# Kernel optimization log

Measured on AMD Instinct MI355X. Metric: run time of the kernel, lower is better.

Reference implementation:

```python
import jax, jax.numpy as jnp
import numpy as np

N_HEAD = 16
N_KV_GROUP = 4
WINDOW = 256


def setup_inputs() -> dict:
    key = jax.random.key(0)
    ks = jax.random.split(key, 5)
    B, T, C = 2, 2048, 1024
    KV = C // N_HEAD * N_KV_GROUP  # 256
    s = 0.02
    return {
        "x": jax.random.normal(ks[0], (B, T, C), jnp.float32),
        "Wq": jax.random.normal(ks[1], (C, C), jnp.float32) * s,
        "bq": jnp.zeros((C,), jnp.float32),
        "Wk": jax.random.normal(ks[2], (C, KV), jnp.float32) * s,
        "bk": jnp.zeros((KV,), jnp.float32),
        "Wv": jax.random.normal(ks[3], (C, KV), jnp.float32) * s,
        "bv": jnp.zeros((KV,), jnp.float32),
        "Wo": jax.random.normal(ks[4], (C, C), jnp.float32) * s,
        "bo": jnp.zeros((C,), jnp.float32),
    }


def reference(x, Wq, bq, Wk, bk, Wv, bv, Wo, bo):
    B, T, C = x.shape
    hd = C // N_HEAD  # head dim = 64
    n_rep = N_HEAD // N_KV_GROUP

    q = x @ Wq + bq                      # [B,T,C]
    k = x @ Wk + bk                      # [B,T,KV]
    v = x @ Wv + bv

    q = q.reshape(B, T, N_HEAD, hd).transpose(0, 2, 1, 3)       # [B,H,T,d]
    k = k.reshape(B, T, N_KV_GROUP, hd).transpose(0, 2, 1, 3)   # [B,G,T,d]
    v = v.reshape(B, T, N_KV_GROUP, hd).transpose(0, 2, 1, 3)

    # GQA: repeat_interleave kv heads along head dim
    k_rep = jnp.repeat(k, n_rep, axis=1)                         # [B,H,T,d]
    v_rep = jnp.repeat(v, n_rep, axis=1)

    att = jnp.einsum("bhqd,bhkd->bhqk", q, k_rep) / jnp.sqrt(jnp.float32(hd))

    # causal + sliding window band mask: q position i attends to j in [i-WINDOW, i]
    i = jnp.arange(T)[:, None]
    j = jnp.arange(T)[None, :]
    band = (j <= i) & (j >= i - WINDOW)                           # [T,T]
    att = jnp.where(band[None, None], att, jnp.float32(-jnp.inf))

    att = jax.nn.softmax(att, axis=-1)
    y = jnp.einsum("bhqk,bhkd->bhqd", att, v_rep)                 # [B,H,T,d]
    y = y.transpose(0, 2, 1, 3).reshape(B, T, C)
    return y @ Wo + bo
```

## Files before the change

kernel.cpp:

```cpp
#include <hip/hip_runtime.h>
#include <hip/hip_bf16.h>

#define TT 2048
#define CC 1024
#define KVD 256
#define QKVD 1536

typedef __bf16 bf16x8 __attribute__((ext_vector_type(8)));
typedef float f32x4 __attribute__((ext_vector_type(4)));

__device__ __forceinline__ void gload_lds16(const __hip_bfloat16* g, __hip_bfloat16* l) {
  __builtin_amdgcn_global_load_lds(
      (const __attribute__((address_space(1))) unsigned int*)g,
      (__attribute__((address_space(3))) unsigned int*)l, 16, 0, 0);
}


__global__ __launch_bounds__(256) void k_prep(const float* __restrict__ x,
                                              const float* __restrict__ Wq,
                                              const float* __restrict__ Wk,
                                              const float* __restrict__ Wv,
                                              const float* __restrict__ Wo,
                                              const float* __restrict__ bq,
                                              const float* __restrict__ bk,
                                              const float* __restrict__ bv,
                                              __hip_bfloat16* __restrict__ xbf,
                                              __hip_bfloat16* __restrict__ wqkvT,
                                              __hip_bfloat16* __restrict__ woT,
                                              float* __restrict__ bqkv) {
  const int bxid = blockIdx.x;
  if (bxid < 4096) {
    size_t idx = ((size_t)bxid * 256 + threadIdx.x) * 4;
    float4 v = *(const float4*)(x + idx);
    xbf[idx + 0] = __float2bfloat16(v.x);
    xbf[idx + 1] = __float2bfloat16(v.y);
    xbf[idx + 2] = __float2bfloat16(v.z);
    xbf[idx + 3] = __float2bfloat16(v.w);
    return;
  }
  if (bxid == 4736) {
    for (int i = threadIdx.x; i < 1536; i += 256) {
      float v;
      if (i < 1024)      v = bq[i];
      else if (i < 1280) v = bk[i - 1024];
      else               v = bv[i - 1280];
      bqkv[i] = v;
    }
    return;
  }
  __shared__ float tile[64][65];
  const float* src;
  int ncols, k0, n0;
  __hip_bfloat16* dst;
  if (bxid < 4480) {
    const int idx = bxid - 4096;
    k0 = (idx & 15) * 64;
    n0 = (idx >> 4) * 64;
    dst = wqkvT;
    if (n0 < 1024)      { src = Wq; ncols = 1024; }
    else if (n0 < 1280) { src = Wk - 1024; ncols = 256; }
    else                { src = Wv - 1280; ncols = 256; }
  } else {
    const int idx = bxid - 4480;
    k0 = (idx & 15) * 64;
    n0 = (idx >> 4) * 64;
    dst = woT; src = Wo; ncols = 1024;
  }
  const int rw = threadIdx.x >> 6;
  const int cl = threadIdx.x & 63;
#pragma unroll
  for (int i = 0; i < 16; ++i) {
    const int kr = rw + i * 4;
    tile[kr][cl] = src[(size_t)(k0 + kr) * ncols + n0 + cl];
  }
  __syncthreads();
#pragma unroll
  for (int i = 0; i < 16; ++i) {
    const int nr = rw + i * 4;
    dst[(size_t)(n0 + nr) * 1024 + k0 + cl] = __float2bfloat16(tile[cl][nr]);
  }
}


__global__ __launch_bounds__(256, 3) void k_gemm1(const __hip_bfloat16* __restrict__ A,
                                                  const __hip_bfloat16* __restrict__ BT,
                                                  const float* __restrict__ bias,
                                                  __hip_bfloat16* __restrict__ C,
                                                  __hip_bfloat16* __restrict__ vtg) {
  __shared__ __hip_bfloat16 As[128][64];
  __shared__ __hip_bfloat16 Bs[128][64];

  const int tid  = threadIdx.x;
  const int m0   = blockIdx.y * 128;
  const int n0   = blockIdx.x * 128;
  const int w    = tid >> 6;
  const int lane = tid & 63;
  const int quad = lane >> 4;
  const int l16  = lane & 15;
  const int wm   = (w >> 1) * 64;
  const int wn   = (w & 1) * 64;

  const int dl_r = lane >> 3;
  const int dl_c = (lane & 7) ^ dl_r;

  const __hip_bfloat16* gA = A + (size_t)(m0 + w * 32 + dl_r) * 1024 + dl_c * 8;
  const __hip_bfloat16* gB = BT + (size_t)(n0 + w * 32 + dl_r) * 1024 + dl_c * 8;

  f32x4 acc[4][4] = {};

  for (int kt = 0; kt < 16; ++kt) {
    const int k0 = kt << 6;
#pragma unroll
    for (int rr = 0; rr < 4; ++rr) {
      gload_lds16(gA + k0 + (size_t)(rr * 8) * 1024, &As[w * 32 + rr * 8][0]);
      gload_lds16(gB + k0 + (size_t)(rr * 8) * 1024, &Bs[w * 32 + rr * 8][0]);
    }
    __syncthreads();

#pragma unroll
    for (int ks = 0; ks < 2; ++ks) {
      const int cb = (ks << 2) + quad;
      bf16x8 fa[4], fb[4];
#pragma unroll
      for (int i = 0; i < 4; ++i)
        fa[i] = *(const bf16x8*)&As[wm + i * 16 + l16][(cb ^ (l16 & 7)) << 3];
#pragma unroll
      for (int j = 0; j < 4; ++j)
        fb[j] = *(const bf16x8*)&Bs[wn + j * 16 + l16][(cb ^ (l16 & 7)) << 3];
#pragma unroll
      for (int i = 0; i < 4; ++i)
#pragma unroll
        for (int j = 0; j < 4; ++j)
          acc[i][j] = __builtin_amdgcn_mfma_f32_16x16x32_bf16(fa[i], fb[j], acc[i][j], 0, 0, 0);
    }
    __syncthreads();
  }

#pragma unroll
  for (int j = 0; j < 4; ++j) {
    const int gn = n0 + wn + j * 16 + l16;
    const float bias_v = bias[gn];
    if (gn >= 1280) {
      const int dfull = gn - 1280;
      const int gg = dfull >> 6;
      const int dd = dfull & 63;
#pragma unroll
      for (int i = 0; i < 4; ++i) {
        const int gm = m0 + wm + i * 16 + quad * 4;
        const int bb = gm >> 11;
        const int tl = gm & 2047;
        __hip_bfloat16 tmp[4];
#pragma unroll
        for (int r = 0; r < 4; ++r) tmp[r] = __float2bfloat16(acc[i][j][r] + bias_v);
        *(uint2*)(vtg + ((size_t)((bb * 4 + gg) * 64 + dd)) * TT + tl) = *(const uint2*)tmp;
      }
    } else {
#pragma unroll
      for (int i = 0; i < 4; ++i) {
        const int gmb = m0 + wm + i * 16 + quad * 4;
#pragma unroll
        for (int r = 0; r < 4; ++r)
          C[(size_t)(gmb + r) * QKVD + gn] = __float2bfloat16(acc[i][j][r] + bias_v);
      }
    }
  }
}


__global__ __launch_bounds__(256, 4) void k_gemm2(const __hip_bfloat16* __restrict__ A,
                                                  const __hip_bfloat16* __restrict__ BT,
                                                  const float* __restrict__ bias,
                                                  float* __restrict__ C) {
  __shared__ __hip_bfloat16 As[64][64];
  __shared__ __hip_bfloat16 Bs[128][64];

  const int tid  = threadIdx.x;
  const int m0   = blockIdx.y * 64;
  const int n0   = blockIdx.x * 128;
  const int w    = tid >> 6;
  const int lane = tid & 63;
  const int quad = lane >> 4;
  const int l16  = lane & 15;
  const int wm   = (w >> 1) * 32;
  const int wn   = (w & 1) * 64;

  const int dl_r = lane >> 3;
  const int dl_c = (lane & 7) ^ dl_r;

  const __hip_bfloat16* gA = A + (size_t)(m0 + w * 16 + dl_r) * 1024 + dl_c * 8;
  const __hip_bfloat16* gB = BT + (size_t)(n0 + w * 32 + dl_r) * 1024 + dl_c * 8;

  f32x4 acc[2][4] = {};

  for (int kt = 0; kt < 16; ++kt) {
    const int k0 = kt << 6;
    gload_lds16(gA + k0,                     &As[w * 16][0]);
    gload_lds16(gA + k0 + (size_t)8 * 1024,  &As[w * 16 + 8][0]);
    gload_lds16(gB + k0,                     &Bs[w * 32][0]);
    gload_lds16(gB + k0 + (size_t)8 * 1024,  &Bs[w * 32 + 8][0]);
    gload_lds16(gB + k0 + (size_t)16 * 1024, &Bs[w * 32 + 16][0]);
    gload_lds16(gB + k0 + (size_t)24 * 1024, &Bs[w * 32 + 24][0]);
    __syncthreads();

#pragma unroll
    for (int ks = 0; ks < 2; ++ks) {
      const int cb = (ks << 2) + quad;
      bf16x8 fa[2], fb[4];
#pragma unroll
      for (int i = 0; i < 2; ++i)
        fa[i] = *(const bf16x8*)&As[wm + i * 16 + l16][(cb ^ (l16 & 7)) << 3];
#pragma unroll
      for (int j = 0; j < 4; ++j)
        fb[j] = *(const bf16x8*)&Bs[wn + j * 16 + l16][(cb ^ (l16 & 7)) << 3];
#pragma unroll
      for (int i = 0; i < 2; ++i)
#pragma unroll
        for (int j = 0; j < 4; ++j)
          acc[i][j] = __builtin_amdgcn_mfma_f32_16x16x32_bf16(fa[i], fb[j], acc[i][j], 0, 0, 0);
    }
    __syncthreads();
  }

#pragma unroll
  for (int j = 0; j < 4; ++j) {
    const int gn = n0 + wn + j * 16 + l16;
    const float bias_v = bias[gn];
#pragma unroll
    for (int i = 0; i < 2; ++i) {
      const int gmb = m0 + wm + i * 16 + quad * 4;
#pragma unroll
      for (int r = 0; r < 4; ++r)
        C[(size_t)(gmb + r) * CC + gn] = acc[i][j][r] + bias_v;
    }
  }
}


__global__ __launch_bounds__(256) void k_attn(const __hip_bfloat16* __restrict__ qkv,
                                              const __hip_bfloat16* __restrict__ vtg,
                                              __hip_bfloat16* __restrict__ y) {
  __shared__ __hip_bfloat16 Kb[2][64][64];
  __shared__ __hip_bfloat16 Vb[2][64][64];
  __shared__ __hip_bfloat16 Ps[4][16][72];

  const int t    = threadIdx.x;
  const int w    = t >> 6;
  const int lane = t & 63;
  const int quad = lane >> 4;
  const int l16  = lane & 15;
  const int bx   = blockIdx.x;
  const int h    = blockIdx.y;
  const int b    = blockIdx.z;
  const int g    = h >> 2;
  const int i0   = bx * 64;
  const int qrow      = i0 + w * 16 + l16;
  const int my_q_base = i0 + w * 16 + quad * 4;

  const int lrow = lane >> 3;
  const int cgl  = (lane & 7) ^ lrow;

  const __hip_bfloat16* kg =
      qkv + ((size_t)(b * TT + w * 16 + lrow)) * QKVD + 1024 + g * 64 + cgl * 8;
  const __hip_bfloat16* vg =
      vtg + ((size_t)((b * 4 + g) * 64 + w * 16 + lrow)) * TT + cgl * 8;

  bf16x8 fq[2];
  {
    const __hip_bfloat16* qp = qkv + ((size_t)(b * TT + qrow)) * QKVD + h * 64 + quad * 8;
    fq[0] = *(const bf16x8*)qp;
    fq[1] = *(const bf16x8*)(qp + 32);
  }

  float l_r[4] = {0.f, 0.f, 0.f, 0.f};
  f32x4 o_acc[4] = {};
  const float EC = 0.125f * 1.44269504f;

  const int c_lo = bx >= 4 ? bx - 4 : 0;

  {
    const size_t ko = (size_t)(c_lo * 64) * QKVD;
    gload_lds16(kg + ko,                    &Kb[0][w * 16][0]);
    gload_lds16(kg + ko + (size_t)8 * QKVD, &Kb[0][w * 16 + 8][0]);
    const int vo = c_lo * 64;
    gload_lds16(vg + vo,                  &Vb[0][w * 16][0]);
    gload_lds16(vg + vo + (size_t)8 * TT, &Vb[0][w * 16 + 8][0]);
  }

  int buf = 0;
  for (int c = c_lo; c <= bx; ++c) {
    __syncthreads();
    if (c < bx) {
      const size_t ko = (size_t)((c + 1) * 64) * QKVD;
      gload_lds16(kg + ko,                    &Kb[buf ^ 1][w * 16][0]);
      gload_lds16(kg + ko + (size_t)8 * QKVD, &Kb[buf ^ 1][w * 16 + 8][0]);
      const int vo = (c + 1) * 64;
      gload_lds16(vg + vo,                  &Vb[buf ^ 1][w * 16][0]);
      gload_lds16(vg + vo + (size_t)8 * TT, &Vb[buf ^ 1][w * 16 + 8][0]);
    }

    const int jc = c * 64;

    f32x4 sacc[4] = {};
#pragma unroll
    for (int ks = 0; ks < 2; ++ks) {
      const int sw = (((ks << 2) + quad) ^ (l16 & 7)) << 3;
#pragma unroll
      for (int nt = 0; nt < 4; ++nt) {
        const bf16x8 fk = *(const bf16x8*)&Kb[buf][nt * 16 + l16][sw];
        sacc[nt] = __builtin_amdgcn_mfma_f32_16x16x32_bf16(fq[ks], fk, sacc[nt], 0, 0, 0);
      }
    }

    if (c == bx) {
#pragma unroll
      for (int r = 0; r < 4; ++r) {
        const int gi = my_q_base + r;
#pragma unroll
        for (int nt = 0; nt < 4; ++nt) {
          const int key = jc + nt * 16 + l16;
          const float p = (key <= gi) ? exp2f(sacc[nt][r] * EC) : 0.f;
          l_r[r] += p;
          Ps[w][quad * 4 + r][nt * 16 + l16] = __float2bfloat16(p);
        }
      }
    } else if (bx >= 4 && c == c_lo) {
#pragma unroll
      for (int r = 0; r < 4; ++r) {
        const int glo = my_q_base + r - 256;
#pragma unroll
        for (int nt = 0; nt < 4; ++nt) {
          const int key = jc + nt * 16 + l16;
          const float p = (key >= glo) ? exp2f(sacc[nt][r] * EC) : 0.f;
          l_r[r] += p;
          Ps[w][quad * 4 + r][nt * 16 + l16] = __float2bfloat16(p);
        }
      }
    } else {
#pragma unroll
      for (int r = 0; r < 4; ++r)
#pragma unroll
        for (int nt = 0; nt < 4; ++nt) {
          const float p = exp2f(sacc[nt][r] * EC);
          l_r[r] += p;
          Ps[w][quad * 4 + r][nt * 16 + l16] = __float2bfloat16(p);
        }
    }

    const bf16x8 fp0 = *(const bf16x8*)&Ps[w][l16][quad * 8];
    const bf16x8 fp1 = *(const bf16x8*)&Ps[w][l16][32 + quad * 8];

#pragma unroll
    for (int ks = 0; ks < 2; ++ks) {
      const int sw = (((ks << 2) + quad) ^ (l16 & 7)) << 3;
#pragma unroll
      for (int jt = 0; jt < 4; ++jt) {
        const bf16x8 fv = *(const bf16x8*)&Vb[buf][jt * 16 + l16][sw];
        o_acc[jt] = __builtin_amdgcn_mfma_f32_16x16x32_bf16(ks == 0 ? fp0 : fp1, fv,
                                                            o_acc[jt], 0, 0, 0);
      }
    }
    buf ^= 1;
  }

#pragma unroll
  for (int r = 0; r < 4; ++r) {
#pragma unroll
    for (int d = 1; d < 16; d <<= 1) l_r[r] += __shfl_xor(l_r[r], d);
    const float inv = 1.f / l_r[r];
    __hip_bfloat16* yp = y + ((size_t)(b * TT + my_q_base + r)) * CC + h * 64 + l16;
#pragma unroll
    for (int jt = 0; jt < 4; ++jt)
      yp[jt * 16] = __float2bfloat16(o_acc[jt][r] * inv);
  }
}


extern "C" void kernel_launch(void* const* d_in, const int* in_sizes, int n_in,
                              void* d_out, int out_size, void* d_ws, size_t ws_size,
                              hipStream_t stream) {
  const float* x  = (const float*)d_in[0];
  const float* Wq = (const float*)d_in[1];
  const float* bq = (const float*)d_in[2];
  const float* Wk = (const float*)d_in[3];
  const float* bk = (const float*)d_in[4];
  const float* Wv = (const float*)d_in[5];
  const float* bv = (const float*)d_in[6];
  const float* Wo = (const float*)d_in[7];
  const float* bo = (const float*)d_in[8];
  float* out = (float*)d_out;

  char* ws = (char*)d_ws;
  const size_t M = 2 * TT;
  __hip_bfloat16* xbf   = (__hip_bfloat16*)(ws);
  __hip_bfloat16* qkv   = (__hip_bfloat16*)(ws + 8388608);
  __hip_bfloat16* ybf   = (__hip_bfloat16*)(ws + 20971520);
  __hip_bfloat16* wqkvT = (__hip_bfloat16*)(ws + 29360128);
  __hip_bfloat16* woT   = (__hip_bfloat16*)(ws + 32505856);
  float*          bqkv  = (float*)(ws + 34603008);
  __hip_bfloat16* vtg   = (__hip_bfloat16*)(ws + 34609152);

  k_prep<<<4737, 256, 0, stream>>>(x, Wq, Wk, Wv, Wo, bq, bk, bv,
                                   xbf, wqkvT, woT, bqkv);

  k_gemm1<<<dim3(QKVD / 128, M / 128), 256, 0, stream>>>(xbf, wqkvT, bqkv, qkv, vtg);

  k_attn<<<dim3(TT / 64, 16, 2), 256, 0, stream>>>(qkv, vtg, ybf);

  k_gemm2<<<dim3(CC / 128, M / 64), 256, 0, stream>>>(ybf, woT, bo, out);
}
```

Before: 145.1 us.

## Process 128 queries per attention block to reuse K/V tiles across two subtiles

The attention kernel now covers 128 query rows per block: each wave handles two 16-row subtiles that share the same K/V tiles in shared memory, which halves the K/V global traffic per query. Subtiles whose rows lie entirely outside the band for the current key chunk are skipped, and the mask logic is merged into a single causal-plus-window check. It also adds a min-blocks-per-CU hint of 3. The trade-off is that the grid halves to 512 blocks, each wave holds more registers, and each block walks more chunks, so less parallelism is available.

Measured after the change: 146.8 us. About the same (+1.1%).

```diff
diff --git a/kernel.cpp b/kernel.cpp
--- a/kernel.cpp
+++ b/kernel.cpp
@@ -236,12 +236,12 @@
 }
 
 
-__global__ __launch_bounds__(256) void k_attn(const __hip_bfloat16* __restrict__ qkv,
-                                              const __hip_bfloat16* __restrict__ vtg,
-                                              __hip_bfloat16* __restrict__ y) {
+__global__ __launch_bounds__(256, 3) void k_attn(const __hip_bfloat16* __restrict__ qkv,
+                                                 const __hip_bfloat16* __restrict__ vtg,
+                                                 __hip_bfloat16* __restrict__ y) {
   __shared__ __hip_bfloat16 Kb[2][64][64];
   __shared__ __hip_bfloat16 Vb[2][64][64];
-  __shared__ __hip_bfloat16 Ps[4][16][72];
+  __shared__ __hip_bfloat16 Ps[4][32][72];
 
   const int t    = threadIdx.x;
   const int w    = t >> 6;
@@ -252,9 +252,7 @@
   const int h    = blockIdx.y;
   const int b    = blockIdx.z;
   const int g    = h >> 2;
-  const int i0   = bx * 64;
-  const int qrow      = i0 + w * 16 + l16;
-  const int my_q_base = i0 + w * 16 + quad * 4;
+  const int i0   = bx * 128;
 
   const int lrow = lane >> 3;
   const int cgl  = (lane & 7) ^ lrow;
@@ -264,18 +262,21 @@
   const __hip_bfloat16* vg =
       vtg + ((size_t)((b * 4 + g) * 64 + w * 16 + lrow)) * TT + cgl * 8;
 
-  bf16x8 fq[2];
-  {
+  bf16x8 fq[2][2];
+#pragma unroll
+  for (int st = 0; st < 2; ++st) {
+    const int qrow = i0 + w * 32 + st * 16 + l16;
     const __hip_bfloat16* qp = qkv + ((size_t)(b * TT + qrow)) * QKVD + h * 64 + quad * 8;
-    fq[0] = *(const bf16x8*)qp;
-    fq[1] = *(const bf16x8*)(qp + 32);
-  }
-
-  float l_r[4] = {0.f, 0.f, 0.f, 0.f};
-  f32x4 o_acc[4] = {};
+    fq[st][0] = *(const bf16x8*)qp;
+    fq[st][1] = *(const bf16x8*)(qp + 32);
+  }
+
+  float l_r[2][4] = {};
+  f32x4 o_acc[2][4] = {};
   const float EC = 0.125f * 1.44269504f;
 
-  const int c_lo = bx >= 4 ? bx - 4 : 0;
+  const int c_lo = (i0 >= 256) ? ((i0 - 256) >> 6) : 0;
+  const int c_hi = (i0 + 127) >> 6;
 
   {
     const size_t ko = (size_t)(c_lo * 64) * QKVD;
@@ -287,9 +288,9 @@
   }
 
   int buf = 0;
-  for (int c = c_lo; c <= bx; ++c) {
+  for (int c = c_lo; c <= c_hi; ++c) {
     __syncthreads();
-    if (c < bx) {
+    if (c < c_hi) {
       const size_t ko = (size_t)((c + 1) * 64) * QKVD;
       gload_lds16(kg + ko,                    &Kb[buf ^ 1][w * 16][0]);
       gload_lds16(kg + ko + (size_t)8 * QKVD, &Kb[buf ^ 1][w * 16 + 8][0]);
@@ -300,77 +301,79 @@
 
     const int jc = c * 64;
 
-    f32x4 sacc[4] = {};
-#pragma unroll
-    for (int ks = 0; ks < 2; ++ks) {
-      const int sw = (((ks << 2) + quad) ^ (l16 & 7)) << 3;
-#pragma unroll
-      for (int nt = 0; nt < 4; ++nt) {
-        const bf16x8 fk = *(const bf16x8*)&Kb[buf][nt * 16 + l16][sw];
-        sacc[nt] = __builtin_amdgcn_mfma_f32_16x16x32_bf16(fq[ks], fk, sacc[nt], 0, 0, 0);
-      }
-    }
-
-    if (c == bx) {
-#pragma unroll
-      for (int r = 0; r < 4; ++r) {
-        const int gi = my_q_base + r;
+#pragma unroll
+    for (int st = 0; st < 2; ++st) {
+      const int qb = i0 + w * 32 + st * 16;
+      if (jc > qb + 15 || jc + 63 < qb - 256) continue;
+
+      f32x4 sacc[4] = {};
+#pragma unroll
+      for (int ks = 0; ks < 2; ++ks) {
+        const int sw = (((ks << 2) + quad) ^ (l16 & 7)) << 3;
 #pragma unroll
         for (int nt = 0; nt < 4; ++nt) {
-          const int key = jc + nt * 16 + l16;
-          const float p = (key <= gi) ? exp2f(sacc[nt][r] * EC) : 0.f;
-          l_r[r] += p;
-          Ps[w][quad * 4 + r][nt * 16 + l16] = __float2bfloat16(p);
+          const bf16x8 fk = *(const bf16x8*)&Kb[buf][nt * 16 + l16][sw];
+          sacc[nt] = __builtin_amdgcn_mfma_f32_16x16x32_bf16(fq[st][ks], fk, sacc[nt], 0, 0, 0);
         }
       }
-    } else if (bx >= 4 && c == c_lo) {
-#pragma unroll
-      for (int r = 0; r < 4; ++r) {
-        const int glo = my_q_base + r - 256;
-#pragma unroll
-        for (int nt = 0; nt < 4; ++nt) {
-          const int key = jc + nt * 16 + l16;
-          const float p = (key >= glo) ? exp2f(sacc[nt][r] * EC) : 0.f;
-          l_r[r] += p;
-          Ps[w][quad * 4 + r][nt * 16 + l16] = __float2bfloat16(p);
+
+      const bool needC = (jc + 63 > qb);
+      const bool needW = (jc < qb + 15 - 256);
+      if (needC || needW) {
+#pragma unroll
+        for (int r = 0; r < 4; ++r) {
+          const int gi = qb + quad * 4 + r;
+#pragma unroll
+          for (int nt = 0; nt < 4; ++nt) {
+            const int key = jc + nt * 16 + l16;
+            const bool valid = (key <= gi) && (key >= gi - 256);
+            const float p = valid ? exp2f(sacc[nt][r] * EC) : 0.f;
+            l_r[st][r] += p;
+            Ps[w][st * 16 + quad * 4 + r][nt * 16 + l16] = __float2bfloat16(p);
+          }
+        }
+      } else {
+#pragma unroll
+        for (int r = 0; r < 4; ++r)
+#pragma unroll
+          for (int nt = 0; nt < 4; ++nt) {
+            const float p = exp2f(sacc[nt][r] * EC);
+            l_r[st][r] += p;
+            Ps[w][st * 16 + quad * 4 + r][nt * 16 + l16] = __float2bfloat16(p);
+          }
+      }
+
+      const bf16x8 fp0 = *(const bf16x8*)&Ps[w][st * 16 + l16][quad * 8];
+      const bf16x8 fp1 = *(const bf16x8*)&Ps[w][st * 16 + l16][32 + quad * 8];
+
+#pragma unroll
+      for (int ks = 0; ks < 2; ++ks) {
+        const int sw = (((ks << 2) + quad) ^ (l16 & 7)) << 3;
+#pragma unroll
+        for (int jt = 0; jt < 4; ++jt) {
+          const bf16x8 fv = *(const bf16x8*)&Vb[buf][jt * 16 + l16][sw];
+          o_acc[st][jt] = __builtin_amdgcn_mfma_f32_16x16x32_bf16(ks == 0 ? fp0 : fp1, fv,
+                                                                  o_acc[st][jt], 0, 0, 0);
         }
       }
-    } else {
-#pragma unroll
-      for (int r = 0; r < 4; ++r)
-#pragma unroll
-        for (int nt = 0; nt < 4; ++nt) {
-          const float p = exp2f(sacc[nt][r] * EC);
-          l_r[r] += p;
-          Ps[w][quad * 4 + r][nt * 16 + l16] = __float2bfloat16(p);
-        }
-    }
-
-    const bf16x8 fp0 = *(const bf16x8*)&Ps[w][l16][quad * 8];
-    const bf16x8 fp1 = *(const bf16x8*)&Ps[w][l16][32 + quad * 8];
-
-#pragma unroll
-    for (int ks = 0; ks < 2; ++ks) {
-      const int sw = (((ks << 2) + quad) ^ (l16 & 7)) << 3;
-#pragma unroll
-      for (int jt = 0; jt < 4; ++jt) {
-        const bf16x8 fv = *(const bf16x8*)&Vb[buf][jt * 16 + l16][sw];
-        o_acc[jt] = __builtin_amdgcn_mfma_f32_16x16x32_bf16(ks == 0 ? fp0 : fp1, fv,
-                                                            o_acc[jt], 0, 0, 0);
-      }
     }
     buf ^= 1;
   }
 
 #pragma unroll
-  for (int r = 0; r < 4; ++r) {
-#pragma unroll
-    for (int d = 1; d < 16; d <<= 1) l_r[r] += __shfl_xor(l_r[r], d);
-    const float inv = 1.f / l_r[r];
-    __hip_bfloat16* yp = y + ((size_t)(b * TT + my_q_base + r)) * CC + h * 64 + l16;
-#pragma unroll
-    for (int jt = 0; jt < 4; ++jt)
-      yp[jt * 16] = __float2bfloat16(o_acc[jt][r] * inv);
+  for (int st = 0; st < 2; ++st) {
+#pragma unroll
+    for (int r = 0; r < 4; ++r) {
+      float lv = l_r[st][r];
+#pragma unroll
+      for (int d = 1; d < 16; d <<= 1) lv += __shfl_xor(lv, d);
+      const float inv = 1.f / lv;
+      const int row = i0 + w * 32 + st * 16 + quad * 4 + r;
+      __hip_bfloat16* yp = y + ((size_t)(b * TT + row)) * CC + h * 64 + l16;
+#pragma unroll
+      for (int jt = 0; jt < 4; ++jt)
+        yp[jt * 16] = __float2bfloat16(o_acc[st][jt][r] * inv);
+    }
   }
 }
 
@@ -404,7 +407,7 @@
 
   k_gemm1<<<dim3(QKVD / 128, M / 128), 256, 0, stream>>>(xbf, wqkvT, bqkv, qkv, vtg);
 
-  k_attn<<<dim3(TT / 64, 16, 2), 256, 0, stream>>>(qkv, vtg, ybf);
+  k_attn<<<dim3(TT / 128, 16, 2), 256, 0, stream>>>(qkv, vtg, ybf);
 
   k_gemm2<<<dim3(CC / 128, M / 64), 256, 0, stream>>>(ybf, woT, bo, out);
 }
```

## Fuse all four stages into one persistent cooperative kernel with grid syncs

Applied to the files above, without the earlier changes.

Replaces the four separate launches (prep, QKV GEMM, attention, output GEMM) with a single cooperative persistent kernel. Each stage loops over its tiles with a grid-stride loop and is separated from the next by a grid-wide sync, with shared memory held in a union. The aim is to remove per-launch overhead and the idle gaps between kernels. In exchange the grid is capped at 512 blocks with two blocks per CU, so occupancy and tile-level parallelism may drop, and each grid barrier has its own cost. The old multi-kernel path stays as a fallback.

Measured after the change: 427.6 us. 2.95x slower.

```diff
diff --git a/kernel.cpp b/kernel.cpp
--- a/kernel.cpp
+++ b/kernel.cpp
@@ -1,9 +1,11 @@
 #include <hip/hip_runtime.h>
 #include <hip/hip_bf16.h>
+#include <hip/hip_cooperative_groups.h>
+
+namespace cg = cooperative_groups;
 
 #define TT 2048
 #define CC 1024
-#define KVD 256
 #define QKVD 1536
 
 typedef __bf16 bf16x8 __attribute__((ext_vector_type(8)));
@@ -81,7 +83,6 @@
   }
 }
 
-
 __global__ __launch_bounds__(256, 3) void k_gemm1(const __hip_bfloat16* __restrict__ A,
                                                   const __hip_bfloat16* __restrict__ BT,
                                                   const float* __restrict__ bias,
@@ -166,7 +167,6 @@
   }
 }
 
-
 __global__ __launch_bounds__(256, 4) void k_gemm2(const __hip_bfloat16* __restrict__ A,
                                                   const __hip_bfloat16* __restrict__ BT,
                                                   const float* __restrict__ bias,
@@ -234,7 +234,6 @@
     }
   }
 }
-
 
 __global__ __launch_bounds__(256) void k_attn(const __hip_bfloat16* __restrict__ qkv,
                                               const __hip_bfloat16* __restrict__ vtg,
@@ -371,6 +370,353 @@
 #pragma unroll
     for (int jt = 0; jt < 4; ++jt)
       yp[jt * 16] = __float2bfloat16(o_acc[jt][r] * inv);
+  }
+}
+
+
+union SMem {
+  float ptile[64][65];
+  struct { __hip_bfloat16 As[128][64]; __hip_bfloat16 Bs[128][64]; } g1;
+  struct {
+    __hip_bfloat16 Kb[2][64][64];
+    __hip_bfloat16 Vb[2][64][64];
+    __hip_bfloat16 Ps[4][16][72];
+  } at;
+  struct { __hip_bfloat16 As[64][64]; __hip_bfloat16 Bs[128][64]; } g2;
+};
+
+__global__ __launch_bounds__(256, 2) void k_fused(
+    const float* __restrict__ x, const float* __restrict__ Wq, const float* __restrict__ bq,
+    const float* __restrict__ Wk, const float* __restrict__ bk,
+    const float* __restrict__ Wv, const float* __restrict__ bv,
+    const float* __restrict__ Wo, const float* __restrict__ bo,
+    float* __restrict__ out,
+    __hip_bfloat16* __restrict__ xbf, __hip_bfloat16* __restrict__ qkv,
+    __hip_bfloat16* __restrict__ ybf, __hip_bfloat16* __restrict__ wqkvT,
+    __hip_bfloat16* __restrict__ woT, float* __restrict__ bqkv,
+    __hip_bfloat16* __restrict__ vtg) {
+  cg::grid_group gridg = cg::this_grid();
+  __shared__ SMem sm;
+
+  const int tid  = threadIdx.x;
+  const int nblk = gridDim.x;
+  const int w    = tid >> 6;
+  const int lane = tid & 63;
+  const int quad = lane >> 4;
+  const int l16  = lane & 15;
+
+  for (int vb = blockIdx.x; vb < 4737; vb += nblk) {
+    if (vb < 4096) {
+      size_t idx = ((size_t)vb * 256 + tid) * 4;
+      float4 v = *(const float4*)(x + idx);
+      xbf[idx + 0] = __float2bfloat16(v.x);
+      xbf[idx + 1] = __float2bfloat16(v.y);
+      xbf[idx + 2] = __float2bfloat16(v.z);
+      xbf[idx + 3] = __float2bfloat16(v.w);
+    } else if (vb == 4736) {
+      for (int i = tid; i < 1536; i += 256) {
+        float v;
+        if (i < 1024)      v = bq[i];
+        else if (i < 1280) v = bk[i - 1024];
+        else               v = bv[i - 1280];
+        bqkv[i] = v;
+      }
+    } else {
+      const float* src;
+      int ncols, k0, n0;
+      __hip_bfloat16* dst;
+      if (vb < 4480) {
+        const int idx = vb - 4096;
+        k0 = (idx & 15) * 64;
+        n0 = (idx >> 4) * 64;
+        dst = wqkvT;
+        if (n0 < 1024)      { src = Wq; ncols = 1024; }
+        else if (n0 < 1280) { src = Wk - 1024; ncols = 256; }
+        else                { src = Wv - 1280; ncols = 256; }
+      } else {
+        const int idx = vb - 4480;
+        k0 = (idx & 15) * 64;
+        n0 = (idx >> 4) * 64;
+        dst = woT; src = Wo; ncols = 1024;
+      }
+      const int rw = tid >> 6;
+      const int cl = tid & 63;
+      __syncthreads();
+#pragma unroll
+      for (int i = 0; i < 16; ++i) {
+        const int kr = rw + i * 4;
+        sm.ptile[kr][cl] = src[(size_t)(k0 + kr) * ncols + n0 + cl];
+      }
+      __syncthreads();
+#pragma unroll
+      for (int i = 0; i < 16; ++i) {
+        const int nr = rw + i * 4;
+        dst[(size_t)(n0 + nr) * 1024 + k0 + cl] = __float2bfloat16(sm.ptile[cl][nr]);
+      }
+    }
+  }
+  __threadfence();
+  gridg.sync();
+
+  for (int tile = blockIdx.x; tile < 384; tile += nblk) {
+    const int m0 = (tile / 12) * 128;
+    const int n0 = (tile % 12) * 128;
+    const int wm = (w >> 1) * 64;
+    const int wn = (w & 1) * 64;
+    const int dl_r = lane >> 3;
+    const int dl_c = (lane & 7) ^ dl_r;
+
+    const __hip_bfloat16* gA = xbf + (size_t)(m0 + w * 32 + dl_r) * 1024 + dl_c * 8;
+    const __hip_bfloat16* gB = wqkvT + (size_t)(n0 + w * 32 + dl_r) * 1024 + dl_c * 8;
+
+    f32x4 acc[4][4] = {};
+    __syncthreads();
+
+    for (int kt = 0; kt < 16; ++kt) {
+      const int k0 = kt << 6;
+#pragma unroll
+      for (int rr = 0; rr < 4; ++rr) {
+        gload_lds16(gA + k0 + (size_t)(rr * 8) * 1024, &sm.g1.As[w * 32 + rr * 8][0]);
+        gload_lds16(gB + k0 + (size_t)(rr * 8) * 1024, &sm.g1.Bs[w * 32 + rr * 8][0]);
+      }
+      __syncthreads();
+
+#pragma unroll
+      for (int ks = 0; ks < 2; ++ks) {
+        const int cb = (ks << 2) + quad;
+        bf16x8 fa[4], fb[4];
+#pragma unroll
+        for (int i = 0; i < 4; ++i)
+          fa[i] = *(const bf16x8*)&sm.g1.As[wm + i * 16 + l16][(cb ^ (l16 & 7)) << 3];
+#pragma unroll
+        for (int j = 0; j < 4; ++j)
+          fb[j] = *(const bf16x8*)&sm.g1.Bs[wn + j * 16 + l16][(cb ^ (l16 & 7)) << 3];
+#pragma unroll
+        for (int i = 0; i < 4; ++i)
+#pragma unroll
+          for (int j = 0; j < 4; ++j)
+            acc[i][j] = __builtin_amdgcn_mfma_f32_16x16x32_bf16(fa[i], fb[j], acc[i][j], 0, 0, 0);
+      }
+      __syncthreads();
+    }
+
+#pragma unroll
+    for (int j = 0; j < 4; ++j) {
+      const int gn = n0 + wn + j * 16 + l16;
+      const float bias_v = bqkv[gn];
+      if (gn >= 1280) {
+        const int dfull = gn - 1280;
+        const int gg = dfull >> 6;
+        const int dd = dfull & 63;
+#pragma unroll
+        for (int i = 0; i < 4; ++i) {
+          const int gm = m0 + wm + i * 16 + quad * 4;
+          const int bb = gm >> 11;
+          const int tl = gm & 2047;
+          __hip_bfloat16 tmp[4];
+#pragma unroll
+          for (int r = 0; r < 4; ++r) tmp[r] = __float2bfloat16(acc[i][j][r] + bias_v);
+          *(uint2*)(vtg + ((size_t)((bb * 4 + gg) * 64 + dd)) * TT + tl) = *(const uint2*)tmp;
+        }
+      } else {
+#pragma unroll
+        for (int i = 0; i < 4; ++i) {
+          const int gmb = m0 + wm + i * 16 + quad * 4;
+#pragma unroll
+          for (int r = 0; r < 4; ++r)
+            qkv[(size_t)(gmb + r) * QKVD + gn] = __float2bfloat16(acc[i][j][r] + bias_v);
+        }
+      }
+    }
+  }
+  __threadfence();
+  gridg.sync();
+
+  for (int tile = blockIdx.x; tile < 1024; tile += nblk) {
+    const int bx = tile & 31;
+    const int h  = (tile >> 5) & 15;
+    const int b  = tile >> 9;
+    const int g  = h >> 2;
+    const int i0 = bx * 64;
+    const int qrow      = i0 + w * 16 + l16;
+    const int my_q_base = i0 + w * 16 + quad * 4;
+
+    const int lrow = lane >> 3;
+    const int cgl  = (lane & 7) ^ lrow;
+
+    const __hip_bfloat16* kg =
+        qkv + ((size_t)(b * TT + w * 16 + lrow)) * QKVD + 1024 + g * 64 + cgl * 8;
+    const __hip_bfloat16* vg =
+        vtg + ((size_t)((b * 4 + g) * 64 + w * 16 + lrow)) * TT + cgl * 8;
+
+    bf16x8 fq[2];
+    {
+      const __hip_bfloat16* qp = qkv + ((size_t)(b * TT + qrow)) * QKVD + h * 64 + quad * 8;
+      fq[0] = *(const bf16x8*)qp;
+      fq[1] = *(const bf16x8*)(qp + 32);
+    }
+
+    float l_r[4] = {0.f, 0.f, 0.f, 0.f};
+    f32x4 o_acc[4] = {};
+    const float EC = 0.125f * 1.44269504f;
+
+    const int c_lo = bx >= 4 ? bx - 4 : 0;
+
+    __syncthreads();
+    {
+      const size_t ko = (size_t)(c_lo * 64) * QKVD;
+      gload_lds16(kg + ko,                    &sm.at.Kb[0][w * 16][0]);
+      gload_lds16(kg + ko + (size_t)8 * QKVD, &sm.at.Kb[0][w * 16 + 8][0]);
+      const int vo = c_lo * 64;
+      gload_lds16(vg + vo,                  &sm.at.Vb[0][w * 16][0]);
+      gload_lds16(vg + vo + (size_t)8 * TT, &sm.at.Vb[0][w * 16 + 8][0]);
+    }
+
+    int buf = 0;
+    for (int c = c_lo; c <= bx; ++c) {
+      __syncthreads();
+      if (c < bx) {
+        const size_t ko = (size_t)((c + 1) * 64) * QKVD;
+        gload_lds16(kg + ko,                    &sm.at.Kb[buf ^ 1][w * 16][0]);
+        gload_lds16(kg + ko + (size_t)8 * QKVD, &sm.at.Kb[buf ^ 1][w * 16 + 8][0]);
+        const int vo = (c + 1) * 64;
+        gload_lds16(vg + vo,                  &sm.at.Vb[buf ^ 1][w * 16][0]);
+        gload_lds16(vg + vo + (size_t)8 * TT, &sm.at.Vb[buf ^ 1][w * 16 + 8][0]);
+      }
+
+      const int jc = c * 64;
+
+      f32x4 sacc[4] = {};
+#pragma unroll
+      for (int ks = 0; ks < 2; ++ks) {
+        const int sw = (((ks << 2) + quad) ^ (l16 & 7)) << 3;
+#pragma unroll
+        for (int nt = 0; nt < 4; ++nt) {
+          const bf16x8 fk = *(const bf16x8*)&sm.at.Kb[buf][nt * 16 + l16][sw];
+          sacc[nt] = __builtin_amdgcn_mfma_f32_16x16x32_bf16(fq[ks], fk, sacc[nt], 0, 0, 0);
+        }
+      }
+
+      if (c == bx) {
+#pragma unroll
+        for (int r = 0; r < 4; ++r) {
+          const int gi = my_q_base + r;
+#pragma unroll
+          for (int nt = 0; nt < 4; ++nt) {
+            const int key = jc + nt * 16 + l16;
+            const float p = (key <= gi) ? exp2f(sacc[nt][r] * EC) : 0.f;
+            l_r[r] += p;
+            sm.at.Ps[w][quad * 4 + r][nt * 16 + l16] = __float2bfloat16(p);
+          }
+        }
+      } else if (bx >= 4 && c == c_lo) {
+#pragma unroll
+        for (int r = 0; r < 4; ++r) {
+          const int glo = my_q_base + r - 256;
+#pragma unroll
+          for (int nt = 0; nt < 4; ++nt) {
+            const int key = jc + nt * 16 + l16;
+            const float p = (key >= glo) ? exp2f(sacc[nt][r] * EC) : 0.f;
+            l_r[r] += p;
+            sm.at.Ps[w][quad * 4 + r][nt * 16 + l16] = __float2bfloat16(p);
+          }
+        }
+      } else {
+#pragma unroll
+        for (int r = 0; r < 4; ++r)
+#pragma unroll
+          for (int nt = 0; nt < 4; ++nt) {
+            const float p = exp2f(sacc[nt][r] * EC);
+            l_r[r] += p;
+            sm.at.Ps[w][quad * 4 + r][nt * 16 + l16] = __float2bfloat16(p);
+          }
+      }
+
+      const bf16x8 fp0 = *(const bf16x8*)&sm.at.Ps[w][l16][quad * 8];
+      const bf16x8 fp1 = *(const bf16x8*)&sm.at.Ps[w][l16][32 + quad * 8];
+
+#pragma unroll
+      for (int ks = 0; ks < 2; ++ks) {
+        const int sw = (((ks << 2) + quad) ^ (l16 & 7)) << 3;
+#pragma unroll
+        for (int jt = 0; jt < 4; ++jt) {
+          const bf16x8 fv = *(const bf16x8*)&sm.at.Vb[buf][jt * 16 + l16][sw];
+          o_acc[jt] = __builtin_amdgcn_mfma_f32_16x16x32_bf16(ks == 0 ? fp0 : fp1, fv,
+                                                              o_acc[jt], 0, 0, 0);
+        }
+      }
+      buf ^= 1;
+    }
+
+#pragma unroll
+    for (int r = 0; r < 4; ++r) {
+#pragma unroll
+      for (int d = 1; d < 16; d <<= 1) l_r[r] += __shfl_xor(l_r[r], d);
+      const float inv = 1.f / l_r[r];
+      __hip_bfloat16* yp = ybf + ((size_t)(b * TT + my_q_base + r)) * CC + h * 64 + l16;
+#pragma unroll
+      for (int jt = 0; jt < 4; ++jt)
+        yp[jt * 16] = __float2bfloat16(o_acc[jt][r] * inv);
+    }
+  }
+  __threadfence();
+  gridg.sync();
+
+  for (int tile = blockIdx.x; tile < 512; tile += nblk) {
+    const int m0 = (tile >> 3) * 64;
+    const int n0 = (tile & 7) * 128;
+    const int wm = (w >> 1) * 32;
+    const int wn = (w & 1) * 64;
+    const int dl_r = lane >> 3;
+    const int dl_c = (lane & 7) ^ dl_r;
+
+    const __hip_bfloat16* gA = ybf + (size_t)(m0 + w * 16 + dl_r) * 1024 + dl_c * 8;
+    const __hip_bfloat16* gB = woT + (size_t)(n0 + w * 32 + dl_r) * 1024 + dl_c * 8;
+
+    f32x4 acc[2][4] = {};
+    __syncthreads();
+
+    for (int kt = 0; kt < 16; ++kt) {
+      const int k0 = kt << 6;
+      gload_lds16(gA + k0,                     &sm.g2.As[w * 16][0]);
+      gload_lds16(gA + k0 + (size_t)8 * 1024,  &sm.g2.As[w * 16 + 8][0]);
+      gload_lds16(gB + k0,                     &sm.g2.Bs[w * 32][0]);
+      gload_lds16(gB + k0 + (size_t)8 * 1024,  &sm.g2.Bs[w * 32 + 8][0]);
+      gload_lds16(gB + k0 + (size_t)16 * 1024, &sm.g2.Bs[w * 32 + 16][0]);
+      gload_lds16(gB + k0 + (size_t)24 * 1024, &sm.g2.Bs[w * 32 + 24][0]);
+      __syncthreads();
+
+#pragma unroll
+      for (int ks = 0; ks < 2; ++ks) {
+        const int cb = (ks << 2) + quad;
+        bf16x8 fa[2], fb[4];
+#pragma unroll
+        for (int i = 0; i < 2; ++i)
+          fa[i] = *(const bf16x8*)&sm.g2.As[wm + i * 16 + l16][(cb ^ (l16 & 7)) << 3];
+#pragma unroll
+        for (int j = 0; j < 4; ++j)
+          fb[j] = *(const bf16x8*)&sm.g2.Bs[wn + j * 16 + l16][(cb ^ (l16 & 7)) << 3];
+#pragma unroll
+        for (int i = 0; i < 2; ++i)
+#pragma unroll
+          for (int j = 0; j < 4; ++j)
+            acc[i][j] = __builtin_amdgcn_mfma_f32_16x16x32_bf16(fa[i], fb[j], acc[i][j], 0, 0, 0);
+      }
+      __syncthreads();
+    }
+
+#pragma unroll
+    for (int j = 0; j < 4; ++j) {
+      const int gn = n0 + wn + j * 16 + l16;
+      const float bias_v = bo[gn];
+#pragma unroll
+      for (int i = 0; i < 2; ++i) {
+        const int gmb = m0 + wm + i * 16 + quad * 4;
+#pragma unroll
+        for (int r = 0; r < 4; ++r)
+          out[(size_t)(gmb + r) * CC + gn] = acc[i][j][r] + bias_v;
+      }
+    }
   }
 }
 
@@ -399,12 +745,34 @@
   float*          bqkv  = (float*)(ws + 34603008);
   __hip_bfloat16* vtg   = (__hip_bfloat16*)(ws + 34609152);
 
-  k_prep<<<4737, 256, 0, stream>>>(x, Wq, Wk, Wv, Wo, bq, bk, bv,
-                                   xbf, wqkvT, woT, bqkv);
-
-  k_gemm1<<<dim3(QKVD / 128, M / 128), 256, 0, stream>>>(xbf, wqkvT, bqkv, qkv, vtg);
-
-  k_attn<<<dim3(TT / 64, 16, 2), 256, 0, stream>>>(qkv, vtg, ybf);
-
-  k_gemm2<<<dim3(CC / 128, M / 64), 256, 0, stream>>>(ybf, woT, bo, out);
+  int dev = 0;
+  (void)hipGetDevice(&dev);
+  int coop = 0;
+  (void)hipDeviceGetAttribute(&coop, hipDeviceAttributeCooperativeLaunch, dev);
+  int numCU = 0;
+  (void)hipDeviceGetAttribute(&numCU, hipDeviceAttributeMultiprocessorCount, dev);
+  int nb = 0;
+  (void)hipOccupancyMaxActiveBlocksPerMultiprocessor(&nb, k_fused, 256, 0);
+  const long cap = (long)nb * (long)numCU;
+
+  bool done = false;
+  if (coop && cap >= 128) {
+    int grid = (int)(cap < 512 ? cap : 512);
+    void* args[] = {(void*)&x,  (void*)&Wq, (void*)&bq, (void*)&Wk, (void*)&bk,
+                    (void*)&Wv, (void*)&bv, (void*)&Wo, (void*)&bo, (void*)&out,
+                    (void*)&xbf, (void*)&qkv, (void*)&ybf, (void*)&wqkvT,
+                    (void*)&woT, (void*)&bqkv, (void*)&vtg};
+    hipError_t err = hipLaunchCooperativeKernel((const void*)k_fused, dim3(grid),
+                                                dim3(256), args, 0, stream);
+    if (err == hipSuccess) done = true;
+    else (void)hipGetLastError();
+  }
+
+  if (!done) {
+    k_prep<<<4737, 256, 0, stream>>>(x, Wq, Wk, Wv, Wo, bq, bk, bv,
+                                     xbf, wqkvT, woT, bqkv);
+    k_gemm1<<<dim3(QKVD / 128, M / 128), 256, 0, stream>>>(xbf, wqkvT, bqkv, qkv, vtg);
+    k_attn<<<dim3(TT / 64, 16, 2), 256, 0, stream>>>(qkv, vtg, ybf);
+    k_gemm2<<<dim3(CC / 128, M / 64), 256, 0, stream>>>(ybf, woT, bo, out);
+  }
 }
```
